# Performance work log

Measured on AMD Instinct MI355X. Metric: run time of the kernel, lower is better.

## Reference

```python
import jax, jax.numpy as jnp
import numpy as np

LN_EPS = 1e-5

def setup_inputs() -> dict:
    key = jax.random.key(0)
    ks = jax.random.split(key, 4)
    B, N, D, De = 4, 2048, 128, 8
    h = jax.random.normal(ks[0], (B, N, D), dtype=jnp.float32)
    e = jax.random.normal(ks[1], (B, N, N, De), dtype=jnp.float32)
    W_w = jax.random.normal(ks[2], (D, D), dtype=jnp.float32) * (1.0 / np.sqrt(D))
    W_b = jax.random.normal(ks[3], (D,), dtype=jnp.float32) * 0.02
    ln_g = jnp.ones((D,), dtype=jnp.float32)
    ln_b = jnp.zeros((D,), dtype=jnp.float32)
    return {"h": h, "e": e, "W_w": W_w, "W_b": W_b, "ln_g": ln_g, "ln_b": ln_b}

def _layernorm(x, g, b):
    mu = jnp.mean(x, axis=-1, keepdims=True)
    var = jnp.var(x, axis=-1, keepdims=True)
    return (x - mu) * jax.lax.rsqrt(var + LN_EPS) * g + b

def reference(h, e, W_w, W_b, ln_g, ln_b):
    # w_ij = softmax_j(||e_ij||)  -> [B, N, N]
    scores = jnp.linalg.norm(e, axis=-1)          # [B, N, N]
    w = jax.nn.softmax(scores, axis=2)            # softmax over neighbor dim j
    # agg_i = sum_j w_ij * h_j  (batched matmul instead of O(B N^2 D) broadcast)
    agg = jnp.einsum('bij,bjd->bid', w, h)        # [B, N, D]
    z = (h + agg) @ W_w.T + W_b                   # Linear
    h_new = jax.nn.relu(_layernorm(z, ln_g, ln_b)) + h
    return (h_new, e)
```

## Files before the change

### kernel.cpp

```cpp
#include <hip/hip_runtime.h>
#include <hip/hip_bf16.h>
#include <math.h>

constexpr int B  = 4;
constexpr int N  = 2048;
constexpr int D  = 128;
constexpr int De = 8;
constexpr int KS = 8;
constexpr float LN_EPS = 1e-5f;

typedef __bf16 bf16x8 __attribute__((ext_vector_type(8)));
typedef float  f32x4v __attribute__((ext_vector_type(4)));

__device__ inline ushort f2bf(float f) {
    uint u = __float_as_uint(f);
    return (ushort)((u + 0x7fffu + ((u >> 16) & 1u)) >> 16);
}

__global__ __launch_bounds__(256) void k_escore(const float* __restrict__ e,
                                                float* __restrict__ out_e,
                                                uint* __restrict__ w32) {
    const float4* src = reinterpret_cast<const float4*>(e);
    float4*       dst = reinterpret_cast<float4*>(out_e);
    long long base = (long long)blockIdx.x * 1024;
    int t = threadIdx.x;

    #pragma unroll
    for (int p = 0; p < 4; ++p) {
        long long i4 = base + p * 256 + t;
        float4 v = src[i4];
        dst[i4] = v;
        float ss = v.x * v.x + v.y * v.y + v.z * v.z + v.w * v.w;
        ss += __shfl_xor(ss, 1);
        float val = __expf(sqrtf(ss));
        uint bf = f2bf(val);
        uint partner = (uint)__shfl_xor((int)bf, 2);
        if ((t & 3) == 0)
            w32[i4 >> 2] = bf | (partner << 16);
    }
}

__global__ __launch_bounds__(256) void k_hcast(const float* __restrict__ h,
                                               ushort* __restrict__ hT16) {
    __shared__ float tile[32][33];
    int b  = blockIdx.z;
    int n0 = blockIdx.x * 32, d0 = blockIdx.y * 32;
    int t  = threadIdx.x;
    int r = t >> 3, c = (t & 7) * 4;
    float4 v = *reinterpret_cast<const float4*>(h + ((long long)b * N + n0 + r) * D + d0 + c);
    tile[r][c] = v.x; tile[r][c + 1] = v.y; tile[r][c + 2] = v.z; tile[r][c + 3] = v.w;
    __syncthreads();
    ushort4 o;
    o.x = f2bf(tile[c + 0][r]);
    o.y = f2bf(tile[c + 1][r]);
    o.z = f2bf(tile[c + 2][r]);
    o.w = f2bf(tile[c + 3][r]);
    *reinterpret_cast<ushort4*>(hT16 + ((long long)b * D + d0 + r) * N + n0 + c) = o;
}

__global__ __launch_bounds__(256) void k_rowsum(const ushort* __restrict__ w16,
                                                float* __restrict__ inv_rowsum) {
    __shared__ float red[4];
    long long row = blockIdx.x;
    int t = threadIdx.x;
    uint4 v = *reinterpret_cast<const uint4*>(w16 + row * (long long)N + t * 8);
    uint u[4] = {v.x, v.y, v.z, v.w};
    float s = 0.0f;
    #pragma unroll
    for (int q = 0; q < 4; ++q) {
        s += __uint_as_float(u[q] << 16);
        s += __uint_as_float(u[q] & 0xffff0000u);
    }
    #pragma unroll
    for (int off = 32; off > 0; off >>= 1) s += __shfl_xor(s, off);
    if ((t & 63) == 0) red[t >> 6] = s;
    __syncthreads();
    if (t == 0)
        inv_rowsum[row] = 1.0f / (red[0] + red[1] + red[2] + red[3]);
}

__global__ __launch_bounds__(256) void k_agg(const ushort* __restrict__ w16,
                                             const ushort* __restrict__ hT16,
                                             float* __restrict__ aggp) {
    constexpr int BM = 64;
    constexpr int BK = 32;
    constexpr int KC = N / KS;
    __shared__ ushort A_s[BM][40];
    __shared__ ushort B_s[D][40];

    int b  = blockIdx.y;
    int i0 = blockIdx.x * BM;
    int kbase = blockIdx.z * KC;
    int t  = threadIdx.x;
    int wid = t >> 6, lane = t & 63;
    int wr = wid >> 1, wc = wid & 1;
    int lr = lane & 15, lk = (lane >> 4) * 8;

    const ushort* wb = w16 + ((long long)b * N + i0) * N + kbase;
    const ushort* hb = hT16 + (long long)b * D * N + kbase;

    f32x4v acc[2][4] = {};

    int ar = t >> 2, ac = (t & 3) * 8;
    int q1 = t + 256;

    uint4 av  = *reinterpret_cast<const uint4*>(wb + (long long)ar * N + ac);
    uint4 bv0 = *reinterpret_cast<const uint4*>(hb + (long long)(t >> 2) * N + (t & 3) * 8);
    uint4 bv1 = *reinterpret_cast<const uint4*>(hb + (long long)(q1 >> 2) * N + (q1 & 3) * 8);

    for (int k0 = 0; k0 < KC; k0 += BK) {
        __syncthreads();
        *reinterpret_cast<uint4*>(&A_s[ar][ac]) = av;
        *reinterpret_cast<uint4*>(&B_s[t >> 2][(t & 3) * 8]) = bv0;
        *reinterpret_cast<uint4*>(&B_s[q1 >> 2][(q1 & 3) * 8]) = bv1;
        __syncthreads();

        int kn = k0 + BK;
        if (kn < KC) {
            av  = *reinterpret_cast<const uint4*>(wb + (long long)ar * N + kn + ac);
            bv0 = *reinterpret_cast<const uint4*>(hb + (long long)(t >> 2) * N + kn + (t & 3) * 8);
            bv1 = *reinterpret_cast<const uint4*>(hb + (long long)(q1 >> 2) * N + kn + (q1 & 3) * 8);
        }

        bf16x8 af[2], bfr[4];
        #pragma unroll
        for (int fm = 0; fm < 2; ++fm)
            af[fm] = *reinterpret_cast<const bf16x8*>(&A_s[wr * 32 + fm * 16 + lr][lk]);
        #pragma unroll
        for (int fn = 0; fn < 4; ++fn)
            bfr[fn] = *reinterpret_cast<const bf16x8*>(&B_s[wc * 64 + fn * 16 + lr][lk]);
        #pragma unroll
        for (int fm = 0; fm < 2; ++fm)
            #pragma unroll
            for (int fn = 0; fn < 4; ++fn)
                acc[fm][fn] = __builtin_amdgcn_mfma_f32_16x16x32_bf16(
                    af[fm], bfr[fn], acc[fm][fn], 0, 0, 0);
    }

    float* ap = aggp + (long long)blockIdx.z * B * N * D + ((long long)b * N + i0) * D;
    #pragma unroll
    for (int fm = 0; fm < 2; ++fm)
        #pragma unroll
        for (int fn = 0; fn < 4; ++fn)
            #pragma unroll
            for (int r = 0; r < 4; ++r) {
                int row = wr * 32 + fm * 16 + (lane >> 4) * 4 + r;
                int col = wc * 64 + fn * 16 + lr;
                ap[(long long)row * D + col] = acc[fm][fn][r];
            }
}

__global__ __launch_bounds__(128) void k_out(const float* __restrict__ h,
                                             const float* __restrict__ aggp,
                                             const float* __restrict__ inv_rowsum,
                                             const float* __restrict__ Ww,
                                             const float* __restrict__ Wb,
                                             const float* __restrict__ ln_g,
                                             const float* __restrict__ ln_b,
                                             float* __restrict__ out) {
    __shared__ __align__(16) float x_s[D];
    __shared__ float red[4];
    constexpr long long BND = (long long)B * N * D;

    long long row = blockIdx.x;
    int d = threadIdx.x;

    float hv = h[row * D + d];
    float a = 0.0f;
    #pragma unroll
    for (int s = 0; s < KS; ++s)
        a += aggp[s * BND + row * D + d];
    a *= inv_rowsum[row];
    x_s[d] = hv + a;
    __syncthreads();

    const float4* wrow = reinterpret_cast<const float4*>(Ww + (long long)d * D);
    const float4* xv   = reinterpret_cast<const float4*>(x_s);
    float z = 0.0f;
    #pragma unroll
    for (int k = 0; k < D / 4; ++k) {
        float4 wv = wrow[k];
        float4 vv = xv[k];
        z += wv.x * vv.x + wv.y * vv.y + wv.z * vv.z + wv.w * vv.w;
    }
    z += Wb[d];

    float s = z;
    #pragma unroll
    for (int off = 32; off > 0; off >>= 1) s += __shfl_xor(s, off);
    if ((d & 63) == 0) red[d >> 6] = s;
    __syncthreads();
    float mu = (red[0] + red[1]) * (1.0f / (float)D);
    __syncthreads();

    float dev = z - mu;
    float s2 = dev * dev;
    #pragma unroll
    for (int off = 32; off > 0; off >>= 1) s2 += __shfl_xor(s2, off);
    if ((d & 63) == 0) red[d >> 6] = s2;
    __syncthreads();
    float var = (red[0] + red[1]) * (1.0f / (float)D);

    float y = dev * rsqrtf(var + LN_EPS) * ln_g[d] + ln_b[d];
    out[row * D + d] = fmaxf(y, 0.0f) + hv;
}

extern "C" void kernel_launch(void* const* d_in, const int* in_sizes, int n_in,
                              void* d_out, int out_size, void* d_ws, size_t ws_size,
                              hipStream_t stream) {
    const float* h    = (const float*)d_in[0];
    const float* e    = (const float*)d_in[1];
    const float* Ww   = (const float*)d_in[2];
    const float* Wb   = (const float*)d_in[3];
    const float* ln_g = (const float*)d_in[4];
    const float* ln_b = (const float*)d_in[5];

    float* out   = (float*)d_out;
    float* out_h = out;
    float* out_e = out + (size_t)B * N * D;

    ushort* w16  = (ushort*)d_ws;
    ushort* hT16 = w16 + (size_t)B * N * N;
    float*  aggp = (float*)(hT16 + (size_t)B * D * N);
    float*  inv_rowsum = aggp + (size_t)KS * B * N * D;

    long long total_f4 = (long long)B * N * N * De / 4;
    int eblocks = (int)(total_f4 / 1024);

    k_escore<<<eblocks, 256, 0, stream>>>(e, out_e, (uint*)w16);
    dim3 gh(N / 32, D / 32, B);
    k_hcast<<<gh, 256, 0, stream>>>(h, hT16);
    k_rowsum<<<B * N, 256, 0, stream>>>(w16, (float*)inv_rowsum);
    dim3 g2(N / 64, B, KS);
    k_agg<<<g2, 256, 0, stream>>>(w16, hT16, aggp);
    k_out<<<B * N, 128, 0, stream>>>(h, aggp, inv_rowsum, Ww, Wb, ln_g, ln_b, out_h);
}
```

Baseline: 290.1 us.

## Fuse edge-score computation and row sums into the aggregation GEMM kernel

Computes exp(||e_ij||) directly inside the aggregation kernel while staging the A tile in shared memory. This removes the bf16 score matrix round-trip through global memory and the separate escore and rowsum kernels. Row sums are accumulated in fp32 per K-split and combined in the output kernel. The cost is that the kernel no longer prefetches the next tile into registers, so the e loads sit on the critical path between barriers, and the e copy to the output now happens inside the GEMM loop.

```diff
diff --git a/kernel.cpp b/kernel.cpp
--- a/kernel.cpp
+++ b/kernel.cpp
@@ -15,29 +15,6 @@
 __device__ inline ushort f2bf(float f) {
     uint u = __float_as_uint(f);
     return (ushort)((u + 0x7fffu + ((u >> 16) & 1u)) >> 16);
-}
-
-__global__ __launch_bounds__(256) void k_escore(const float* __restrict__ e,
-                                                float* __restrict__ out_e,
-                                                uint* __restrict__ w32) {
-    const float4* src = reinterpret_cast<const float4*>(e);
-    float4*       dst = reinterpret_cast<float4*>(out_e);
-    long long base = (long long)blockIdx.x * 1024;
-    int t = threadIdx.x;
-
-    #pragma unroll
-    for (int p = 0; p < 4; ++p) {
-        long long i4 = base + p * 256 + t;
-        float4 v = src[i4];
-        dst[i4] = v;
-        float ss = v.x * v.x + v.y * v.y + v.z * v.z + v.w * v.w;
-        ss += __shfl_xor(ss, 1);
-        float val = __expf(sqrtf(ss));
-        uint bf = f2bf(val);
-        uint partner = (uint)__shfl_xor((int)bf, 2);
-        if ((t & 3) == 0)
-            w32[i4 >> 2] = bf | (partner << 16);
-    }
 }
 
 __global__ __launch_bounds__(256) void k_hcast(const float* __restrict__ h,
@@ -58,30 +35,11 @@
     *reinterpret_cast<ushort4*>(hT16 + ((long long)b * D + d0 + r) * N + n0 + c) = o;
 }
 
-__global__ __launch_bounds__(256) void k_rowsum(const ushort* __restrict__ w16,
-                                                float* __restrict__ inv_rowsum) {
-    __shared__ float red[4];
-    long long row = blockIdx.x;
-    int t = threadIdx.x;
-    uint4 v = *reinterpret_cast<const uint4*>(w16 + row * (long long)N + t * 8);
-    uint u[4] = {v.x, v.y, v.z, v.w};
-    float s = 0.0f;
-    #pragma unroll
-    for (int q = 0; q < 4; ++q) {
-        s += __uint_as_float(u[q] << 16);
-        s += __uint_as_float(u[q] & 0xffff0000u);
-    }
-    #pragma unroll
-    for (int off = 32; off > 0; off >>= 1) s += __shfl_xor(s, off);
-    if ((t & 63) == 0) red[t >> 6] = s;
-    __syncthreads();
-    if (t == 0)
-        inv_rowsum[row] = 1.0f / (red[0] + red[1] + red[2] + red[3]);
-}
-
-__global__ __launch_bounds__(256) void k_agg(const ushort* __restrict__ w16,
-                                             const ushort* __restrict__ hT16,
-                                             float* __restrict__ aggp) {
+__global__ __launch_bounds__(256) void k_agg_fused(const float* __restrict__ e,
+                                                   float* __restrict__ out_e,
+                                                   const ushort* __restrict__ hT16,
+                                                   float* __restrict__ aggp,
+                                                   float* __restrict__ partial) {
     constexpr int BM = 64;
     constexpr int BK = 32;
     constexpr int KC = N / KS;
@@ -96,31 +54,41 @@
     int wr = wid >> 1, wc = wid & 1;
     int lr = lane & 15, lk = (lane >> 4) * 8;
 
-    const ushort* wb = w16 + ((long long)b * N + i0) * N + kbase;
+    int r = t >> 2, l4 = t & 3;
+    const float4* esrc = reinterpret_cast<const float4*>(e);
+    float4*       edst = reinterpret_cast<float4*>(out_e);
+    long long erow = (((long long)b * N + i0 + r) * N + kbase) * 2;
+
     const ushort* hb = hT16 + (long long)b * D * N + kbase;
+    int hd = t >> 1, hoff = (t & 1) * 16;
 
     f32x4v acc[2][4] = {};
-
-    int ar = t >> 2, ac = (t & 3) * 8;
-    int q1 = t + 256;
-
-    uint4 av  = *reinterpret_cast<const uint4*>(wb + (long long)ar * N + ac);
-    uint4 bv0 = *reinterpret_cast<const uint4*>(hb + (long long)(t >> 2) * N + (t & 3) * 8);
-    uint4 bv1 = *reinterpret_cast<const uint4*>(hb + (long long)(q1 >> 2) * N + (q1 & 3) * 8);
+    float rowacc = 0.0f;
 
     for (int k0 = 0; k0 < KC; k0 += BK) {
         __syncthreads();
-        *reinterpret_cast<uint4*>(&A_s[ar][ac]) = av;
-        *reinterpret_cast<uint4*>(&B_s[t >> 2][(t & 3) * 8]) = bv0;
-        *reinterpret_cast<uint4*>(&B_s[q1 >> 2][(q1 & 3) * 8]) = bv1;
+
+        uint4 hv0 = *reinterpret_cast<const uint4*>(hb + (long long)hd * N + k0 + hoff);
+        uint4 hv1 = *reinterpret_cast<const uint4*>(hb + (long long)hd * N + k0 + hoff + 8);
+        *reinterpret_cast<uint4*>(&B_s[hd][hoff])     = hv0;
+        *reinterpret_cast<uint4*>(&B_s[hd][hoff + 8]) = hv1;
+
+        #pragma unroll
+        for (int q = 0; q < 16; ++q) {
+            long long i4 = erow + k0 * 2 + l4 + 4 * q;
+            float4 v = esrc[i4];
+            edst[i4] = v;
+            float ss = v.x * v.x + v.y * v.y + v.z * v.z + v.w * v.w;
+            ss += __shfl_xor(ss, 1);
+            float val = __expf(sqrtf(ss));
+            rowacc += val;
+            uint bf = f2bf(val);
+            uint partner = (uint)__shfl_xor((int)bf, 2);
+            if (l4 == 0)
+                *reinterpret_cast<uint*>(&A_s[r][2 * q]) = bf | (partner << 16);
+        }
+
         __syncthreads();
-
-        int kn = k0 + BK;
-        if (kn < KC) {
-            av  = *reinterpret_cast<const uint4*>(wb + (long long)ar * N + kn + ac);
-            bv0 = *reinterpret_cast<const uint4*>(hb + (long long)(t >> 2) * N + kn + (t & 3) * 8);
-            bv1 = *reinterpret_cast<const uint4*>(hb + (long long)(q1 >> 2) * N + kn + (q1 & 3) * 8);
-        }
 
         bf16x8 af[2], bfr[4];
         #pragma unroll
@@ -137,22 +105,27 @@
                     af[fm], bfr[fn], acc[fm][fn], 0, 0, 0);
     }
 
+    rowacc += __shfl_xor(rowacc, 1);
+    rowacc += __shfl_xor(rowacc, 2);
+    if (l4 == 0)
+        partial[(long long)blockIdx.z * (B * N) + (long long)b * N + i0 + r] = rowacc * 0.5f;
+
     float* ap = aggp + (long long)blockIdx.z * B * N * D + ((long long)b * N + i0) * D;
     #pragma unroll
     for (int fm = 0; fm < 2; ++fm)
         #pragma unroll
         for (int fn = 0; fn < 4; ++fn)
             #pragma unroll
-            for (int r = 0; r < 4; ++r) {
-                int row = wr * 32 + fm * 16 + (lane >> 4) * 4 + r;
+            for (int rr = 0; rr < 4; ++rr) {
+                int row = wr * 32 + fm * 16 + (lane >> 4) * 4 + rr;
                 int col = wc * 64 + fn * 16 + lr;
-                ap[(long long)row * D + col] = acc[fm][fn][r];
+                ap[(long long)row * D + col] = acc[fm][fn][rr];
             }
 }
 
 __global__ __launch_bounds__(128) void k_out(const float* __restrict__ h,
                                              const float* __restrict__ aggp,
-                                             const float* __restrict__ inv_rowsum,
+                                             const float* __restrict__ partial,
                                              const float* __restrict__ Ww,
                                              const float* __restrict__ Wb,
                                              const float* __restrict__ ln_g,
@@ -161,6 +134,7 @@
     __shared__ __align__(16) float x_s[D];
     __shared__ float red[4];
     constexpr long long BND = (long long)B * N * D;
+    constexpr long long BN  = (long long)B * N;
 
     long long row = blockIdx.x;
     int d = threadIdx.x;
@@ -170,7 +144,11 @@
     #pragma unroll
     for (int s = 0; s < KS; ++s)
         a += aggp[s * BND + row * D + d];
-    a *= inv_rowsum[row];
+    float psum = 0.0f;
+    #pragma unroll
+    for (int s = 0; s < KS; ++s)
+        psum += partial[s * BN + row];
+    a *= (1.0f / psum);
     x_s[d] = hv + a;
     __syncthreads();
 
@@ -219,19 +197,13 @@
     float* out_h = out;
     float* out_e = out + (size_t)B * N * D;
 
-    ushort* w16  = (ushort*)d_ws;
-    ushort* hT16 = w16 + (size_t)B * N * N;
+    ushort* hT16 = (ushort*)d_ws;
     float*  aggp = (float*)(hT16 + (size_t)B * D * N);
-    float*  inv_rowsum = aggp + (size_t)KS * B * N * D;
-
-    long long total_f4 = (long long)B * N * N * De / 4;
-    int eblocks = (int)(total_f4 / 1024);
-
-    k_escore<<<eblocks, 256, 0, stream>>>(e, out_e, (uint*)w16);
+    float*  partial = aggp + (size_t)KS * B * N * D;
+
     dim3 gh(N / 32, D / 32, B);
     k_hcast<<<gh, 256, 0, stream>>>(h, hT16);
-    k_rowsum<<<B * N, 256, 0, stream>>>(w16, (float*)inv_rowsum);
     dim3 g2(N / 64, B, KS);
-    k_agg<<<g2, 256, 0, stream>>>(w16, hT16, aggp);
-    k_out<<<B * N, 128, 0, stream>>>(h, aggp, inv_rowsum, Ww, Wb, ln_g, ln_b, out_h);
-}
+    k_agg_fused<<<g2, 256, 0, stream>>>(e, out_e, hT16, aggp, partial);
+    k_out<<<B * N, 128, 0, stream>>>(h, aggp, partial, Ww, Wb, ln_g, ln_b, out_h);
+}
```

After: 443.2 us. 1.53x slower.
